# Kernel optimization log

Hardware: AMD Instinct MI355X
Metric: run time of the kernel (lower is better)

## Reference

```python
import jax, jax.numpy as jnp
import numpy as np
from jax import lax

B, S, H, A = 8, 2048, 16, 128   # batch, seq, num_head, i_head_dim
D = 128                          # o_head_dim
LN_EPS = 1e-6


def setup_inputs() -> dict:
    key = jax.random.key(0)
    ks = jax.random.split(key, 6)
    heads_input = jax.random.normal(ks[0], (B, S, H, A), dtype=jnp.float32)
    # grouped linear weights: (heads, in_per_head, out_per_head)
    w_hid = jax.random.normal(ks[1], (H, 2 * A, 3 * D), dtype=jnp.float32) * 0.02
    b_hid = jnp.zeros((H, 3 * D), dtype=jnp.float32)
    w_og = jax.random.normal(ks[2], (H, A + D, D), dtype=jnp.float32) * 0.02
    b_og = jnp.zeros((H, D), dtype=jnp.float32)
    ln_g = jnp.ones((H, A), dtype=jnp.float32)
    ln_b = jnp.zeros((H, A), dtype=jnp.float32)
    init_cx = jnp.zeros((H, D), dtype=jnp.float32)
    return {"heads_input": heads_input, "w_hid": w_hid, "b_hid": b_hid,
            "w_og": w_og, "b_og": b_og, "ln_g": ln_g, "ln_b": ln_b,
            "init_cx": init_cx}


def _ln2d(x, g, b):
    # LayerNorm over the last two dims (H, A)
    m = jnp.mean(x, axis=(-2, -1), keepdims=True)
    v = jnp.var(x, axis=(-2, -1), keepdims=True)
    return (x - m) * lax.rsqrt(v + LN_EPS) * g + b


def _forward(heads_input, w_hid, b_hid, w_og, b_og, ln_g, ln_b, init_cx):
    # cumulative-sum + LayerNorm (RS1cumsumstatnorm, states=None)
    csum = _ln2d(jnp.cumsum(heads_input, axis=1), ln_g, ln_b)  # (B,S,H,A)
    # grouped (per-head) linear: 2A -> 3D
    hid_in = jnp.concatenate([heads_input, csum], axis=-1)     # (B,S,H,2A)
    gates = jnp.einsum('bshi,hio->bsho', hid_in, w_hid) + b_hid  # (B,S,H,3D)
    igate, fgate, hidden = jnp.split(gates, 3, axis=-1)
    fgate = jax.nn.sigmoid(fgate)
    hidden = jax.nn.relu(hidden)
    igh = jax.nn.sigmoid(igate) * hidden                        # (B,S,H,D)
    # forget-gated linear recurrence c_t = f_t * c_{t-1} + igh_t (LGateFunc)
    def combine(c1, c2):
        a1, u1 = c1
        a2, u2 = c2
        return a1 * a2, u1 * a2 + u2
    F, C = lax.associative_scan(combine, (fgate, igh), axis=1)
    cell = C + F * init_cx[None, None]                          # (B,S,H,D)
    # output gate: grouped linear (A+D -> D), sigmoid, gate the cell
    og_in = jnp.concatenate([heads_input, cell], axis=-1)       # (B,S,H,A+D)
    og = jax.nn.sigmoid(jnp.einsum('bshi,hio->bsho', og_in, w_og) + b_og)
    return og * cell


def reference(heads_input, w_hid, b_hid, w_og, b_og, ln_g, ln_b, init_cx):
    return _forward(heads_input, w_hid, b_hid, w_og, b_og, ln_g, ln_b, init_cx)
```

## Files before the change

kernel.cpp:

```cpp
#include <hip/hip_runtime.h>
#include <stdint.h>

#define Bb 8
#define Ss 2048
#define Hh 16
#define Aa 128
#define Dd 128
#define NGATE 384
#define KDIM 256
#define NCH 16
#define CLEN 128
#define ROWS (Bb*Ss)
#define ROWSTR (Hh*Aa)

typedef float f32x4 __attribute__((ext_vector_type(4)));
typedef __bf16 bf16x8 __attribute__((ext_vector_type(8)));
typedef unsigned short u16x8 __attribute__((ext_vector_type(8)));

static __device__ __forceinline__ unsigned short f2bf(float f){
  unsigned int u = __builtin_bit_cast(unsigned int, f);
  u += 0x7FFFu + ((u >> 16) & 1u);
  return (unsigned short)(u >> 16);
}
static __device__ __forceinline__ float bf2f(unsigned short s){
  unsigned int u = ((unsigned int)s) << 16;
  return __builtin_bit_cast(float, u);
}
static __device__ __forceinline__ float sigf(float x){ return 1.0f/(1.0f + __expf(-x)); }

__global__ void k_conv_whid(const float* __restrict__ w, unsigned short* __restrict__ wt){
  int idx = blockIdx.x*256 + threadIdx.x;
  const int total = Hh*KDIM*NGATE;
  for (; idx < total; idx += gridDim.x*256){
    int o = idx % NGATE; int k = (idx/NGATE) % KDIM; int h = idx/(NGATE*KDIM);
    int g = o >> 7, d = o & 127;
    int nh = d >> 6, dl = d & 63;
    int wn = dl >> 4, ln15 = d & 15;
    int ks = k >> 5, lq = (k >> 3) & 3, kb = k & 7;
    int hy = h*2 + nh;
    int l = lq*16 + ln15;
    size_t dst = (size_t)hy*(192*KDIM) + (size_t)((((wn*8 + ks)*3 + g)*64 + l)*8 + kb);
    wt[dst] = f2bf(w[idx]);
  }
}
__global__ void k_conv_wog(const float* __restrict__ w, unsigned short* __restrict__ wt){
  int idx = blockIdx.x*256 + threadIdx.x;
  const int total = Hh*KDIM*Dd;
  for (; idx < total; idx += gridDim.x*256){
    int o = idx % Dd; int k = (idx/Dd) % KDIM; int h = idx/(Dd*KDIM);
    wt[(size_t)h*(Dd*KDIM) + o*KDIM + k] = f2bf(w[idx]);
  }
}

__global__ void k_cumsum_a(const float* __restrict__ x, float* __restrict__ totals,
                           unsigned short* __restrict__ xbf){
  int c = blockIdx.x;
  int k = c % NCH; int hb = c / NCH;
  int b = hb / Hh, h = hb % Hh;
  int a = threadIdx.x;
  const size_t base = ((size_t)(b*Ss + k*CLEN)*Hh + h)*Aa + a;
  const float* p = x + base;
  unsigned short* xq = xbf + base;
  float run = 0.f;
  #pragma unroll 2
  for (int i = 0; i < CLEN; ++i){
    float v = p[(size_t)i*ROWSTR];
    run += v;
    xq[(size_t)i*ROWSTR] = f2bf(v);
  }
  totals[(size_t)c*Aa + a] = run;
}

__global__ void k_cumsum_c(const unsigned short* __restrict__ xbf, const float* __restrict__ totals,
                           unsigned short* __restrict__ csum){
  int c = blockIdx.x;
  int k = c % NCH; int hb = c / NCH;
  int b = hb / Hh, h = hb % Hh;
  int a = threadIdx.x;
  const float* tp = totals + (size_t)hb*NCH*Aa + a;
  float run = 0.f;
  for (int j = 0; j < k; ++j) run += tp[(size_t)j*Aa];
  const size_t base = ((size_t)(b*Ss + k*CLEN)*Hh + h)*Aa + a;
  const unsigned short* p = xbf + base;
  unsigned short* q = csum + base;
  #pragma unroll 2
  for (int i = 0; i < CLEN; ++i){
    run += bf2f(p[(size_t)i*ROWSTR]);
    q[(size_t)i*ROWSTR] = f2bf(run);
  }
}

__global__ void k_stats(const unsigned short* __restrict__ csum, float2* __restrict__ mr){
  int r = blockIdx.x;
  int t = threadIdx.x;
  const u16x8 v = *(const u16x8*)(csum + (size_t)r*ROWSTR + t*8);
  float s = 0.f, q = 0.f;
  #pragma unroll
  for (int i = 0; i < 8; ++i){ float f = bf2f(v[i]); s += f; q += f*f; }
  #pragma unroll
  for (int off = 32; off; off >>= 1){ s += __shfl_down(s, off); q += __shfl_down(q, off); }
  __shared__ float ls[4], lq[4];
  int wid = t >> 6, lane = t & 63;
  if (lane == 0){ ls[wid] = s; lq[wid] = q; }
  __syncthreads();
  if (t == 0){
    float S2 = ls[0]+ls[1]+ls[2]+ls[3], Q = lq[0]+lq[1]+lq[2]+lq[3];
    float mu = S2 * (1.0f/(float)ROWSTR);
    float var = Q * (1.0f/(float)ROWSTR) - mu*mu;
    mr[r] = make_float2(mu, rsqrtf(var + 1e-6f));
  }
}

#define GSRC(kk_) (((kk_) < 2) ? xbf : csum)
#define GCO(kk_)  (((kk_) & 1) * 64)
#define GROWT(t_) ((mg*16 + (t_))*128)
__launch_bounds__(512, 2)
__global__ void k_gates(const unsigned short* __restrict__ xbf,
                        const unsigned short* __restrict__ csum,
                        const float2* __restrict__ mr,
                        const float* __restrict__ ln_g, const float* __restrict__ ln_b,
                        const unsigned short* __restrict__ wht,
                        const float* __restrict__ b_hid, unsigned int* __restrict__ fu){
  __shared__ unsigned short lA[2][128*64];
  const int mg = blockIdx.x, hy = blockIdx.y;
  const int h = hy >> 1, nh = hy & 1;
  const int tid = threadIdx.x;
  const int lane = tid & 63, wid = tid >> 6;
  const int wm = wid & 1, wn = wid >> 1;
  const int ln15 = lane & 15, lq = lane >> 4;
  const int r0 = tid >> 3, q0 = tid & 7;
  const int lwA0 = (r0*128 + q0*16) ^ ((r0 & 7) << 4);
  const int lwA1 = ((r0+64)*128 + q0*16) ^ ((r0 & 7) << 4);

  bf16x8 Bf[8][3];
  {
    const u16x8* bs8 = (const u16x8*)(wht + (size_t)hy*(192*KDIM));
    #pragma unroll
    for (int ks = 0; ks < 8; ++ks)
      #pragma unroll
      for (int g = 0; g < 3; ++g)
        Bf[ks][g] = __builtin_bit_cast(bf16x8, bs8[((wn*8 + ks)*3 + g)*64 + lane]);
  }
  const int dcol = nh*64 + wn*16 + ln15;
  const float big = b_hid[h*NGATE + dcol];
  const float bfg = b_hid[h*NGATE + 128 + dcol];
  const float bhd = b_hid[h*NGATE + 256 + dcol];

  f32x4 acc[4][3];
  #pragma unroll
  for (int i = 0; i < 4; ++i)
    #pragma unroll
    for (int j = 0; j < 3; ++j) acc[i][j] = (f32x4){0.f,0.f,0.f,0.f};

  u16x8 pa0, pa1;

#define GA_FETCH(t_, kk_) do { \
    const unsigned short* as_ = GSRC(kk_); \
    const size_t base_ = (size_t)(GROWT(t_) + r0)*ROWSTR + h*Aa + GCO(kk_) + q0*8; \
    pa0 = *(const u16x8*)(as_ + base_); \
    pa1 = *(const u16x8*)(as_ + base_ + (size_t)64*ROWSTR); \
  } while(0)
#define GA_WRITE(t_, kk_, buf_) do { \
    if ((kk_) >= 2){ \
      float2 m0_ = mr[GROWT(t_) + r0]; \
      float2 m1_ = mr[GROWT(t_) + r0 + 64]; \
      const float* g_  = ln_g + h*Aa + GCO(kk_) + q0*8; \
      const float* bz_ = ln_b + h*Aa + GCO(kk_) + q0*8; \
      u16x8 o0_, o1_; \
      _Pragma("unroll") \
      for (int i_ = 0; i_ < 8; ++i_){ \
        float gg_ = g_[i_], bb_ = bz_[i_]; \
        o0_[i_] = f2bf((bf2f(pa0[i_]) - m0_.x)*m0_.y*gg_ + bb_); \
        o1_[i_] = f2bf((bf2f(pa1[i_]) - m1_.x)*m1_.y*gg_ + bb_); \
      } \
      *(u16x8*)((char*)lA[buf_] + lwA0) = o0_; \
      *(u16x8*)((char*)lA[buf_] + lwA1) = o1_; \
    } else { \
      *(u16x8*)((char*)lA[buf_] + lwA0) = pa0; \
      *(u16x8*)((char*)lA[buf_] + lwA1) = pa1; \
    } \
  } while(0)

  GA_FETCH(0, 0); GA_WRITE(0, 0, 0);
  GA_FETCH(0, 1);

  for (int t = 0; t < 16; ++t){
    #pragma unroll
    for (int kk = 0; kk < 4; ++kk){
      const int cur = kk & 1;
      __syncthreads();
      if (kk < 3){
        GA_WRITE(t, kk+1, cur^1);
        if (kk + 2 < 4) GA_FETCH(t, kk+2);
        else if (t + 1 < 16) GA_FETCH(t+1, 0);
      } else {
        if (t + 1 < 16){
          GA_WRITE(t+1, 0, cur^1);
          GA_FETCH(t+1, 1);
        }
      }
      #pragma unroll
      for (int ks2 = 0; ks2 < 2; ++ks2){
        const int kel = ks2*32 + lq*8;
        bf16x8 af[4];
        #pragma unroll
        for (int mf = 0; mf < 4; ++mf){
          int ra = wm*64 + mf*16 + ln15;
          af[mf] = __builtin_bit_cast(bf16x8,
            *(const u16x8*)((const char*)lA[cur] + ((ra*128 + kel*2) ^ ((ra & 7) << 4))));
        }
        #pragma unroll
        for (int g = 0; g < 3; ++g)
          #pragma unroll
          for (int mf = 0; mf < 4; ++mf)
            acc[mf][g] = __builtin_amdgcn_mfma_f32_16x16x32_bf16(
                af[mf], Bf[kk*2 + ks2][g], acc[mf][g], 0, 0, 0);
      }
      if (kk == 3){
        const int m0 = GROWT(t);
        #pragma unroll
        for (int mf = 0; mf < 4; ++mf){
          const int rowb = m0 + wm*64 + mf*16 + lq*4;
          f32x4 aig = acc[mf][0], afg = acc[mf][1], ahd = acc[mf][2];
          #pragma unroll
          for (int r = 0; r < 4; ++r){
            float fg = sigf(afg[r] + bfg);
            float uu = sigf(aig[r] + big) * fmaxf(ahd[r] + bhd, 0.0f);
            fu[(size_t)(rowb + r)*ROWSTR + h*Dd + dcol] =
              ((unsigned int)f2bf(uu) << 16) | (unsigned int)f2bf(fg);
          }
          acc[mf][0] = (f32x4){0.f,0.f,0.f,0.f};
          acc[mf][1] = (f32x4){0.f,0.f,0.f,0.f};
          acc[mf][2] = (f32x4){0.f,0.f,0.f,0.f};
        }
      }
    }
  }
#undef GA_FETCH
#undef GA_WRITE
}

__global__ void k_recur_a(const unsigned int* __restrict__ fu,
                          float* __restrict__ Fc, float* __restrict__ Cc){
  int c = blockIdx.x;
  int k = c % NCH; int hb = c / NCH;
  int b = hb / Hh, h = hb % Hh;
  int d = threadIdx.x;
  const unsigned int* p = fu + ((size_t)(b*Ss + k*CLEN)*Hh + h)*Dd + d;
  float F = 1.f, C = 0.f;
  #pragma unroll 4
  for (int i = 0; i < CLEN; ++i){
    unsigned int v = p[(size_t)i*ROWSTR];
    float f = bf2f((unsigned short)v);
    float u = bf2f((unsigned short)(v >> 16));
    C = fmaf(f, C, u);
    F *= f;
  }
  Fc[(size_t)c*Dd + d] = F;
  Cc[(size_t)c*Dd + d] = C;
}

__global__ void k_recur_b(const float* __restrict__ Fc, const float* __restrict__ Cc,
                          const float* __restrict__ init_cx, float* __restrict__ gcarry){
  int bh = blockIdx.x;
  int h = bh % Hh;
  int d = threadIdx.x;
  float carry = init_cx[h*Dd + d];
  for (int j = 0; j < NCH; ++j){
    size_t o = ((size_t)bh*NCH + j)*Dd + d;
    gcarry[o] = carry;
    carry = fmaf(Fc[o], carry, Cc[o]);
  }
}

#define CPITCH 132
#define XPITCH 136
__launch_bounds__(512, 2)
__global__ void k_og_fused(const unsigned short* __restrict__ xbf,
                           const unsigned int* __restrict__ fu,
                           const unsigned short* __restrict__ wot,
                           const float* __restrict__ gcarry,
                           const float* __restrict__ b_og, float* __restrict__ out){
  __shared__ float s_cell[128*CPITCH];
  __shared__ unsigned short s_xa[128*XPITCH];
  __shared__ float2 s_scan[4*128];
  __shared__ float s_cc[128];
  const int mg = blockIdx.x;
  const int h  = blockIdx.y;
  const int tid = threadIdx.x;
  const int lane = tid & 63, wid = tid >> 6;
  const int wm = wid >> 2, wn = wid & 3;
  const int ln15 = lane & 15, lq = lane >> 4;
  const int rd = tid & 127, rq = tid >> 7;

  bf16x8 Bf[8][2];
  {
    unsigned short* bst = (unsigned short*)s_cell;
    const u16x8* bs = (const u16x8*)(wot + (size_t)h*(Dd*KDIM));
    u16x8* d8 = (u16x8*)bst;
    #pragma unroll
    for (int i = 0; i < 8; ++i) d8[tid + i*512] = bs[tid + i*512];
    if (tid < 128)
      s_cc[tid] = gcarry[((size_t)((mg>>1)*Hh + h)*NCH + (mg & 1)*8)*Dd + tid];
    __syncthreads();
    #pragma unroll
    for (int ks = 0; ks < 8; ++ks)
      #pragma unroll
      for (int j = 0; j < 2; ++j){
        int n = wn*32 + j*16 + ln15;
        Bf[ks][j] = __builtin_bit_cast(bf16x8,
          *(const u16x8*)(bst + n*KDIM + ks*32 + lq*8));
      }
    __syncthreads();
  }

  f32x4 acc[4][2];
  #pragma unroll
  for (int i = 0; i < 4; ++i){ acc[i][0] = (f32x4){0,0,0,0}; acc[i][1] = (f32x4){0,0,0,0}; }

  for (int t = 0; t < 8; ++t){
    const int row0 = (mg*8 + t)*128;
    unsigned int uf[32];
    const unsigned int* fp = fu + (size_t)(row0 + rq*32)*ROWSTR + h*Dd + rd;
    #pragma unroll
    for (int i = 0; i < 32; ++i) uf[i] = fp[(size_t)i*ROWSTR];
    #pragma unroll
    for (int i = 0; i < 4; ++i){
      int c = tid + i*512;
      int r = c >> 4, c8 = c & 15;
      u16x8 v = *(const u16x8*)(xbf + (size_t)(row0 + r)*ROWSTR + h*Aa + c8*8);
      *(u16x8*)&s_xa[r*XPITCH + c8*8] = v;
    }
    float F = 1.f, C = 0.f;
    #pragma unroll
    for (int i = 0; i < 32; ++i){
      float f = bf2f((unsigned short)uf[i]);
      float u = bf2f((unsigned short)(uf[i] >> 16));
      C = fmaf(f, C, u); F *= f;
    }
    s_scan[rq*128 + rd] = make_float2(F, C);
    __syncthreads();
    float cin = s_cc[rd];
    #pragma unroll
    for (int qq = 0; qq < 3; ++qq){
      if (rq > qq){ float2 s = s_scan[qq*128 + rd]; cin = fmaf(s.x, cin, s.y); }
    }
    __syncthreads();
    if (rq == 3){ float2 s3 = s_scan[3*128 + rd]; s_cc[rd] = fmaf(s3.x, cin, s3.y); }
    {
      float c = cin;
      #pragma unroll
      for (int i = 0; i < 32; ++i){
        float f = bf2f((unsigned short)uf[i]);
        float u = bf2f((unsigned short)(uf[i] >> 16));
        c = fmaf(f, c, u);
        s_cell[(rq*32 + i)*CPITCH + rd] = c;
      }
    }
    __syncthreads();
    #pragma unroll
    for (int ks = 0; ks < 4; ++ks){
      bf16x8 af[4];
      #pragma unroll
      for (int mf = 0; mf < 4; ++mf){
        int ra = wm*64 + mf*16 + ln15;
        af[mf] = __builtin_bit_cast(bf16x8,
          *(const u16x8*)&s_xa[ra*XPITCH + ks*32 + lq*8]);
      }
      #pragma unroll
      for (int mf = 0; mf < 4; ++mf)
        #pragma unroll
        for (int j = 0; j < 2; ++j)
          acc[mf][j] = __builtin_amdgcn_mfma_f32_16x16x32_bf16(af[mf], Bf[ks][j], acc[mf][j], 0, 0, 0);
    }
    #pragma unroll
    for (int ks = 4; ks < 8; ++ks){
      bf16x8 af[4];
      #pragma unroll
      for (int mf = 0; mf < 4; ++mf){
        int ra = wm*64 + mf*16 + ln15;
        const float* cp = &s_cell[ra*CPITCH + (ks-4)*32 + lq*8];
        f32x4 c0 = *(const f32x4*)cp;
        f32x4 c1 = *(const f32x4*)(cp + 4);
        u16x8 tt;
        tt[0]=f2bf(c0[0]); tt[1]=f2bf(c0[1]); tt[2]=f2bf(c0[2]); tt[3]=f2bf(c0[3]);
        tt[4]=f2bf(c1[0]); tt[5]=f2bf(c1[1]); tt[6]=f2bf(c1[2]); tt[7]=f2bf(c1[3]);
        af[mf] = __builtin_bit_cast(bf16x8, tt);
      }
      #pragma unroll
      for (int mf = 0; mf < 4; ++mf)
        #pragma unroll
        for (int j = 0; j < 2; ++j)
          acc[mf][j] = __builtin_amdgcn_mfma_f32_16x16x32_bf16(af[mf], Bf[ks][j], acc[mf][j], 0, 0, 0);
    }
    #pragma unroll
    for (int mf = 0; mf < 4; ++mf){
      const int rl = wm*64 + mf*16 + lq*4;
      #pragma unroll
      for (int j = 0; j < 2; ++j){
        const int d = wn*32 + j*16 + ln15;
        const float bo = b_og[h*Dd + d];
        #pragma unroll
        for (int r = 0; r < 4; ++r){
          float cell = s_cell[(rl + r)*CPITCH + d];
          out[(size_t)(row0 + rl + r)*ROWSTR + h*Dd + d] = sigf(acc[mf][j][r] + bo) * cell;
        }
        acc[mf][j] = (f32x4){0.f,0.f,0.f,0.f};
      }
    }
    __syncthreads();
  }
}

extern "C" void kernel_launch(void* const* d_in, const int* in_sizes, int n_in,
                              void* d_out, int out_size, void* d_ws, size_t ws_size,
                              hipStream_t stream){
  const float* x       = (const float*)d_in[0];
  const float* w_hid   = (const float*)d_in[1];
  const float* b_hid   = (const float*)d_in[2];
  const float* w_og    = (const float*)d_in[3];
  const float* b_og    = (const float*)d_in[4];
  const float* ln_g    = (const float*)d_in[5];
  const float* ln_b    = (const float*)d_in[6];
  const float* init_cx = (const float*)d_in[7];
  float* out = (float*)d_out;

  char* ws = (char*)d_ws;
  unsigned short* csum = (unsigned short*)(ws);
  unsigned int*   fu   = (unsigned int*)  (ws + ((size_t)64  << 20));
  unsigned short* xbf  = (unsigned short*)(ws + ((size_t)192 << 20));
  float*          tot  = (float*)         (ws + ((size_t)256 << 20));
  float*          Fc   = (float*)         (ws + ((size_t)257 << 20));
  float*          Cc   = (float*)         (ws + ((size_t)258 << 20));
  float2*         mr   = (float2*)        (ws + ((size_t)259 << 20));
  unsigned short* wht  = (unsigned short*)(ws + ((size_t)260 << 20));
  unsigned short* wot  = (unsigned short*)(ws + ((size_t)263 << 20));
  float*          gcar = (float*)         (ws + ((size_t)264 << 20));

  k_conv_whid<<<2048, 256, 0, stream>>>(w_hid, wht);
  k_conv_wog <<<1024, 256, 0, stream>>>(w_og,  wot);
  k_cumsum_a <<<Bb*Hh*NCH, Aa, 0, stream>>>(x, tot, xbf);
  k_cumsum_c <<<Bb*Hh*NCH, Aa, 0, stream>>>(xbf, tot, csum);
  k_stats    <<<ROWS, 256, 0, stream>>>(csum, mr);
  k_gates    <<<dim3(8, 32), 512, 0, stream>>>(xbf, csum, mr, ln_g, ln_b, wht, b_hid, fu);
  k_recur_a  <<<Bb*Hh*NCH, Dd, 0, stream>>>(fu, Fc, Cc);
  k_recur_b  <<<Bb*Hh, Dd, 0, stream>>>(Fc, Cc, init_cx, gcar);
  k_og_fused <<<dim3(16, 16), 512, 0, stream>>>(xbf, fu, wot, gcar, b_og, out);
}
```

Before: 340.9 us.

## Apply LayerNorm in stats kernel and simplify gates GEMM A-tile pipeline

The stats kernel now normalizes the cumsum rows in place, applying mean/rstd and gamma/beta, and writes bf16 back. This removes the per-element LayerNorm math and the mr lookups from the gates GEMM prologue. The gates kernel now stages full 128-wide K halves (four LDS buffers, two sync points per tile instead of four). The cost is an extra read-modify-write pass over the csum buffer and doubled LDS use in k_gates, which could lower occupancy.

```diff
diff --git a/kernel.cpp b/kernel.cpp
--- a/kernel.cpp
+++ b/kernel.cpp
@@ -90,16 +90,19 @@
   }
 }
 
-__global__ void k_stats(const unsigned short* __restrict__ csum, float2* __restrict__ mr){
+__global__ void k_stats_ln(unsigned short* __restrict__ cs,
+                           const float* __restrict__ ln_g, const float* __restrict__ ln_b){
   int r = blockIdx.x;
   int t = threadIdx.x;
-  const u16x8 v = *(const u16x8*)(csum + (size_t)r*ROWSTR + t*8);
+  unsigned short* p = cs + (size_t)r*ROWSTR + t*8;
+  u16x8 v = *(const u16x8*)p;
   float s = 0.f, q = 0.f;
   #pragma unroll
   for (int i = 0; i < 8; ++i){ float f = bf2f(v[i]); s += f; q += f*f; }
   #pragma unroll
   for (int off = 32; off; off >>= 1){ s += __shfl_down(s, off); q += __shfl_down(q, off); }
   __shared__ float ls[4], lq[4];
+  __shared__ float2 mrs;
   int wid = t >> 6, lane = t & 63;
   if (lane == 0){ ls[wid] = s; lq[wid] = q; }
   __syncthreads();
@@ -107,21 +110,32 @@
     float S2 = ls[0]+ls[1]+ls[2]+ls[3], Q = lq[0]+lq[1]+lq[2]+lq[3];
     float mu = S2 * (1.0f/(float)ROWSTR);
     float var = Q * (1.0f/(float)ROWSTR) - mu*mu;
-    mr[r] = make_float2(mu, rsqrtf(var + 1e-6f));
-  }
-}
-
-#define GSRC(kk_) (((kk_) < 2) ? xbf : csum)
-#define GCO(kk_)  (((kk_) & 1) * 64)
+    mrs = make_float2(mu, rsqrtf(var + 1e-6f));
+  }
+  __syncthreads();
+  float mu = mrs.x, rstd = mrs.y;
+  const float4* g4 = (const float4*)(ln_g + t*8);
+  const float4* b4 = (const float4*)(ln_b + t*8);
+  float4 g0 = g4[0], g1 = g4[1], b0 = b4[0], b1 = b4[1];
+  u16x8 o;
+  o[0] = f2bf((bf2f(v[0]) - mu)*rstd*g0.x + b0.x);
+  o[1] = f2bf((bf2f(v[1]) - mu)*rstd*g0.y + b0.y);
+  o[2] = f2bf((bf2f(v[2]) - mu)*rstd*g0.z + b0.z);
+  o[3] = f2bf((bf2f(v[3]) - mu)*rstd*g0.w + b0.w);
+  o[4] = f2bf((bf2f(v[4]) - mu)*rstd*g1.x + b1.x);
+  o[5] = f2bf((bf2f(v[5]) - mu)*rstd*g1.y + b1.y);
+  o[6] = f2bf((bf2f(v[6]) - mu)*rstd*g1.z + b1.z);
+  o[7] = f2bf((bf2f(v[7]) - mu)*rstd*g1.w + b1.w);
+  *(u16x8*)p = o;
+}
+
 #define GROWT(t_) ((mg*16 + (t_))*128)
 __launch_bounds__(512, 2)
 __global__ void k_gates(const unsigned short* __restrict__ xbf,
-                        const unsigned short* __restrict__ csum,
-                        const float2* __restrict__ mr,
-                        const float* __restrict__ ln_g, const float* __restrict__ ln_b,
+                        const unsigned short* __restrict__ csln,
                         const unsigned short* __restrict__ wht,
                         const float* __restrict__ b_hid, unsigned int* __restrict__ fu){
-  __shared__ unsigned short lA[2][128*64];
+  __shared__ unsigned short lA[4][128*64];
   const int mg = blockIdx.x, hy = blockIdx.y;
   const int h = hy >> 1, nh = hy & 1;
   const int tid = threadIdx.x;
@@ -152,71 +166,58 @@
     #pragma unroll
     for (int j = 0; j < 3; ++j) acc[i][j] = (f32x4){0.f,0.f,0.f,0.f};
 
-  u16x8 pa0, pa1;
-
-#define GA_FETCH(t_, kk_) do { \
-    const unsigned short* as_ = GSRC(kk_); \
-    const size_t base_ = (size_t)(GROWT(t_) + r0)*ROWSTR + h*Aa + GCO(kk_) + q0*8; \
+  u16x8 pa0, pa1, pa2, pa3;
+
+#define GA_FETCH(t_, half_) do { \
+    const unsigned short* as_ = (half_) ? csln : xbf; \
+    const size_t base_ = (size_t)(GROWT(t_) + r0)*ROWSTR + h*Aa + q0*8; \
     pa0 = *(const u16x8*)(as_ + base_); \
     pa1 = *(const u16x8*)(as_ + base_ + (size_t)64*ROWSTR); \
+    pa2 = *(const u16x8*)(as_ + base_ + 64); \
+    pa3 = *(const u16x8*)(as_ + base_ + 64 + (size_t)64*ROWSTR); \
   } while(0)
-#define GA_WRITE(t_, kk_, buf_) do { \
-    if ((kk_) >= 2){ \
-      float2 m0_ = mr[GROWT(t_) + r0]; \
-      float2 m1_ = mr[GROWT(t_) + r0 + 64]; \
-      const float* g_  = ln_g + h*Aa + GCO(kk_) + q0*8; \
-      const float* bz_ = ln_b + h*Aa + GCO(kk_) + q0*8; \
-      u16x8 o0_, o1_; \
-      _Pragma("unroll") \
-      for (int i_ = 0; i_ < 8; ++i_){ \
-        float gg_ = g_[i_], bb_ = bz_[i_]; \
-        o0_[i_] = f2bf((bf2f(pa0[i_]) - m0_.x)*m0_.y*gg_ + bb_); \
-        o1_[i_] = f2bf((bf2f(pa1[i_]) - m1_.x)*m1_.y*gg_ + bb_); \
-      } \
-      *(u16x8*)((char*)lA[buf_] + lwA0) = o0_; \
-      *(u16x8*)((char*)lA[buf_] + lwA1) = o1_; \
-    } else { \
-      *(u16x8*)((char*)lA[buf_] + lwA0) = pa0; \
-      *(u16x8*)((char*)lA[buf_] + lwA1) = pa1; \
-    } \
+#define GA_WRITE(bp_) do { \
+    *(u16x8*)((char*)lA[(bp_)*2+0] + lwA0) = pa0; \
+    *(u16x8*)((char*)lA[(bp_)*2+0] + lwA1) = pa1; \
+    *(u16x8*)((char*)lA[(bp_)*2+1] + lwA0) = pa2; \
+    *(u16x8*)((char*)lA[(bp_)*2+1] + lwA1) = pa3; \
   } while(0)
 
-  GA_FETCH(0, 0); GA_WRITE(0, 0, 0);
+  GA_FETCH(0, 0); GA_WRITE(0);
   GA_FETCH(0, 1);
 
   for (int t = 0; t < 16; ++t){
     #pragma unroll
-    for (int kk = 0; kk < 4; ++kk){
-      const int cur = kk & 1;
+    for (int half = 0; half < 2; ++half){
       __syncthreads();
-      if (kk < 3){
-        GA_WRITE(t, kk+1, cur^1);
-        if (kk + 2 < 4) GA_FETCH(t, kk+2);
-        else if (t + 1 < 16) GA_FETCH(t+1, 0);
-      } else {
-        if (t + 1 < 16){
-          GA_WRITE(t+1, 0, cur^1);
-          GA_FETCH(t+1, 1);
+      if (half == 0){
+        GA_WRITE(1);
+        GA_FETCH(t+1 < 16 ? t+1 : t, 0);
+      } else if (t + 1 < 16){
+        GA_WRITE(0);
+        GA_FETCH(t+1, 1);
+      }
+      #pragma unroll
+      for (int kk2 = 0; kk2 < 2; ++kk2){
+        #pragma unroll
+        for (int ks2 = 0; ks2 < 2; ++ks2){
+          const int kel = ks2*32 + lq*8;
+          bf16x8 af[4];
+          #pragma unroll
+          for (int mf = 0; mf < 4; ++mf){
+            int ra = wm*64 + mf*16 + ln15;
+            af[mf] = __builtin_bit_cast(bf16x8,
+              *(const u16x8*)((const char*)lA[half*2 + kk2] + ((ra*128 + kel*2) ^ ((ra & 7) << 4))));
+          }
+          #pragma unroll
+          for (int g = 0; g < 3; ++g)
+            #pragma unroll
+            for (int mf = 0; mf < 4; ++mf)
+              acc[mf][g] = __builtin_amdgcn_mfma_f32_16x16x32_bf16(
+                  af[mf], Bf[half*4 + kk2*2 + ks2][g], acc[mf][g], 0, 0, 0);
         }
       }
-      #pragma unroll
-      for (int ks2 = 0; ks2 < 2; ++ks2){
-        const int kel = ks2*32 + lq*8;
-        bf16x8 af[4];
-        #pragma unroll
-        for (int mf = 0; mf < 4; ++mf){
-          int ra = wm*64 + mf*16 + ln15;
-          af[mf] = __builtin_bit_cast(bf16x8,
-            *(const u16x8*)((const char*)lA[cur] + ((ra*128 + kel*2) ^ ((ra & 7) << 4))));
-        }
-        #pragma unroll
-        for (int g = 0; g < 3; ++g)
-          #pragma unroll
-          for (int mf = 0; mf < 4; ++mf)
-            acc[mf][g] = __builtin_amdgcn_mfma_f32_16x16x32_bf16(
-                af[mf], Bf[kk*2 + ks2][g], acc[mf][g], 0, 0, 0);
-      }
-      if (kk == 3){
+      if (half == 1){
         const int m0 = GROWT(t);
         #pragma unroll
         for (int mf = 0; mf < 4; ++mf){
@@ -432,7 +433,6 @@
   float*          tot  = (float*)         (ws + ((size_t)256 << 20));
   float*          Fc   = (float*)         (ws + ((size_t)257 << 20));
   float*          Cc   = (float*)         (ws + ((size_t)258 << 20));
-  float2*         mr   = (float2*)        (ws + ((size_t)259 << 20));
   unsigned short* wht  = (unsigned short*)(ws + ((size_t)260 << 20));
   unsigned short* wot  = (unsigned short*)(ws + ((size_t)263 << 20));
   float*          gcar = (float*)         (ws + ((size_t)264 << 20));
@@ -441,8 +441,8 @@
   k_conv_wog <<<1024, 256, 0, stream>>>(w_og,  wot);
   k_cumsum_a <<<Bb*Hh*NCH, Aa, 0, stream>>>(x, tot, xbf);
   k_cumsum_c <<<Bb*Hh*NCH, Aa, 0, stream>>>(xbf, tot, csum);
-  k_stats    <<<ROWS, 256, 0, stream>>>(csum, mr);
-  k_gates    <<<dim3(8, 32), 512, 0, stream>>>(xbf, csum, mr, ln_g, ln_b, wht, b_hid, fu);
+  k_stats_ln <<<ROWS, 256, 0, stream>>>(csum, ln_g, ln_b);
+  k_gates    <<<dim3(8, 32), 512, 0, stream>>>(xbf, csum, wht, b_hid, fu);
   k_recur_a  <<<Bb*Hh*NCH, Dd, 0, stream>>>(fu, Fc, Cc);
   k_recur_b  <<<Bb*Hh, Dd, 0, stream>>>(Fc, Cc, init_cx, gcar);
   k_og_fused <<<dim3(16, 16), 512, 0, stream>>>(xbf, fu, wot, gcar, b_og, out);
```

Measured after the change: 328.4 us. -3.7%, faster.
